# Kernel optimization log

Hardware: AMD Instinct MI355X
Metric: run time of the kernel (lower is better)

Reference implementation:

```python
import jax, jax.numpy as jnp
import numpy as np

E, H, I = 8, 1024, 512          # experts, hidden, moe_intermediate
NG, TKG, TOPK = 4, 2, 4          # n_group, topk_group, num_experts_per_tok
SCALE = 2.5                      # routed_scaling_factor


def _mlp(x, wg, wu, wd):
    # SwiGLU MLP: down(silu(gate(x)) * up(x)), all bias-free
    return (jax.nn.silu(x @ wg) * (x @ wu)) @ wd


def setup_inputs() -> dict:
    key = jax.random.key(0)
    ks = jax.random.split(key, 8)
    s = 0.02
    return {
        "hidden_states": jax.random.normal(ks[0], (32, 256, H), jnp.float32),
        "gate_w": jax.random.normal(ks[1], (E, H), jnp.float32) * np.float32(np.sqrt(2.0 / H)),
        "correction_bias": jnp.zeros((E,), jnp.float32),
        "Wg": jax.random.normal(ks[2], (E, H, I), jnp.float32) * s,
        "Wu": jax.random.normal(ks[3], (E, H, I), jnp.float32) * s,
        "Wd": jax.random.normal(ks[4], (E, I, H), jnp.float32) * s,
        "Wg_s": jax.random.normal(ks[5], (H, I), jnp.float32) * s,
        "Wu_s": jax.random.normal(ks[6], (H, I), jnp.float32) * s,
        "Wd_s": jax.random.normal(ks[7], (I, H), jnp.float32) * s,
    }


def reference(hidden_states, gate_w, correction_bias, Wg, Wu, Wd, Wg_s, Wu_s, Wd_s):
    B, T, _ = hidden_states.shape
    x = hidden_states.reshape(-1, H)                     # [N, H]
    N = x.shape[0]

    # ---- TopkRouter + route_tokens_to_experts (float32 router math) ----
    logits = x @ gate_w.T                                # [N, E]
    scores = jax.nn.sigmoid(logits)
    scores_c = scores + correction_bias                  # scores for choice
    grp = scores_c.reshape(N, NG, E // NG)
    group_scores = jnp.sum(jax.lax.top_k(grp, 2)[0], axis=-1)        # [N, NG]
    grp_idx = jax.lax.top_k(group_scores, TKG)[1]                    # [N, TKG]
    group_mask = jnp.zeros_like(group_scores).at[
        jnp.arange(N)[:, None], grp_idx].set(1.0)                    # [N, NG]
    score_mask = jnp.repeat(group_mask, E // NG, axis=-1) > 0.5      # [N, E]
    scores_for_choice = jnp.where(score_mask, scores_c, 0.0)
    topk_idx = jax.lax.top_k(scores_for_choice, TOPK)[1]             # [N, K]
    topk_w = jnp.take_along_axis(scores, topk_idx, axis=-1)          # [N, K]
    topk_w = topk_w / (jnp.sum(topk_w, axis=-1, keepdims=True) + 1e-20)
    topk_w = topk_w * SCALE

    # ---- DSNaiveMoE: equivalent dense-expert combine ----
    # combine weight per (token, expert); zero for unrouted pairs, so the
    # dense evaluation produces exactly the gather/scatter loop's result.
    cw = jnp.sum(jax.nn.one_hot(topk_idx, E, dtype=topk_w.dtype) * topk_w[..., None], axis=1)  # [N, E]
    g = jnp.einsum('nh,ehi->eni', x, Wg)
    u = jnp.einsum('nh,ehi->eni', x, Wu)
    y = jnp.einsum('eni,eih->enh', jax.nn.silu(g) * u, Wd)           # [E, N, H]
    routed = jnp.einsum('enh,ne->nh', y, cw)                          # [N, H]

    # ---- shared expert on residual input (replaces residual add) ----
    out = routed + _mlp(x, Wg_s, Wu_s, Wd_s)
    return out.reshape(B, T, H)
```

## Files before the change

### kernel.cpp

```cpp
#include <hip/hip_runtime.h>

#define E_ 8
#define H_ 1024
#define I_ 512
#define NE 9
#define NTOK 8192

typedef __bf16 bf16;
typedef __bf16 bf16x8 __attribute__((ext_vector_type(8)));
typedef __bf16 bf16x4 __attribute__((ext_vector_type(4)));
typedef float f32x4 __attribute__((ext_vector_type(4)));

__device__ __forceinline__ void gload16(const bf16* g, bf16* l) {
  __builtin_amdgcn_global_load_lds(
      (const __attribute__((address_space(1))) void*)g,
      (__attribute__((address_space(3))) void*)l,
      16, 0, 0);
}

__global__ __launch_bounds__(256) void convert_kernel(
    const float* __restrict__ x, bf16* __restrict__ xb) {
  int i = blockIdx.x * 256 + threadIdx.x;
  f32x4 v = ((const f32x4*)x)[i];
  bf16x4 o = {(bf16)v.x, (bf16)v.y, (bf16)v.z, (bf16)v.w};
  ((bf16x4*)xb)[i] = o;
}

__global__ __launch_bounds__(256) void router_kernel(
    const float* __restrict__ x, const float* __restrict__ gw,
    const float* __restrict__ bias, int4* __restrict__ topk_e,
    float4* __restrict__ topk_w) {
  int t = threadIdx.x;
  int l = t & 63, w = t >> 6;
  int n = blockIdx.x * 4 + w;
  const f32x4* xr = (const f32x4*)(x + (size_t)n * H_ + l * 16);
  float xv[16];
#pragma unroll
  for (int q = 0; q < 4; q++) {
    f32x4 v = xr[q];
    xv[q * 4 + 0] = v.x; xv[q * 4 + 1] = v.y; xv[q * 4 + 2] = v.z; xv[q * 4 + 3] = v.w;
  }
  float s[E_], sc[E_];
#pragma unroll
  for (int e = 0; e < E_; e++) {
    const f32x4* gr = (const f32x4*)(gw + e * H_ + l * 16);
    float acc = 0.f;
#pragma unroll
    for (int q = 0; q < 4; q++) {
      f32x4 g = gr[q];
      acc += xv[q * 4 + 0] * g.x + xv[q * 4 + 1] * g.y + xv[q * 4 + 2] * g.z + xv[q * 4 + 3] * g.w;
    }
#pragma unroll
    for (int off = 32; off > 0; off >>= 1) acc += __shfl_xor(acc, off, 64);
    float sig = 1.f / (1.f + __expf(-acc));
    s[e] = sig;
    sc[e] = sig + bias[e];
  }
  if (l == 0) {
    float gs[4];
#pragma unroll
    for (int g = 0; g < 4; g++) gs[g] = sc[2 * g] + sc[2 * g + 1];
    int g0 = 0;
    for (int g = 1; g < 4; g++) if (gs[g] > gs[g0]) g0 = g;
    int g1 = -1;
    for (int g = 0; g < 4; g++) {
      if (g == g0) continue;
      if (g1 < 0 || gs[g] > gs[g1]) g1 = g;
    }
    int es[4] = {2 * g0, 2 * g0 + 1, 2 * g1, 2 * g1 + 1};
    float wsum = 1e-20f;
    for (int j = 0; j < 4; j++) wsum += s[es[j]];
    float inv = 2.5f / wsum;
    topk_e[n] = (int4){es[0], es[1], es[2], es[3]};
    topk_w[n] = (float4){s[es[0]] * inv, s[es[1]] * inv, s[es[2]] * inv, s[es[3]] * inv};
  }
}

__global__ __launch_bounds__(256) void compact_kernel(
    const int4* __restrict__ topk_e, const float4* __restrict__ topk_w,
    int* __restrict__ cnt, int* __restrict__ idx, float* __restrict__ cwp) {
  __shared__ int hist[E_];
  __shared__ int base[E_];
  int t = threadIdx.x;
  if (t < E_) hist[t] = 0;
  __syncthreads();
  int n = blockIdx.x * 256 + t;
  int4 e4 = topk_e[n];
  float4 w4 = topk_w[n];
  int le[4] = {e4.x, e4.y, e4.z, e4.w};
  float lw[4] = {w4.x, w4.y, w4.z, w4.w};
  int lpos[4];
#pragma unroll
  for (int j = 0; j < 4; j++) lpos[j] = atomicAdd(&hist[le[j]], 1);
  __syncthreads();
  if (t < E_) base[t] = atomicAdd(&cnt[t], hist[t]);
  __syncthreads();
#pragma unroll
  for (int j = 0; j < 4; j++) {
    int p = base[le[j]] + lpos[j];
    idx[le[j] * NTOK + p] = n;
    cwp[le[j] * NTOK + p] = lw[j];
  }
}

__global__ __launch_bounds__(256) void transpose_kernel(
    const float* __restrict__ Wg, const float* __restrict__ Wu,
    const float* __restrict__ Wd, const float* __restrict__ Wgs,
    const float* __restrict__ Wus, const float* __restrict__ Wds,
    bf16* __restrict__ BgT, bf16* __restrict__ BuT, bf16* __restrict__ WdT) {
  __shared__ bf16 tile[32][33];
  int job = blockIdx.x >> 9;
  int tl = blockIdx.x & 511;
  const float* src;
  bf16* dst;
  int C, dst_ld;
  if (job < 18) {
    int e = job % 9;
    if (job < 9) src = (e < 8) ? Wg + (size_t)e * H_ * I_ : Wgs;
    else         src = (e < 8) ? Wu + (size_t)e * H_ * I_ : Wus;
    dst = ((job < 9) ? BgT : BuT) + (size_t)e * I_ * H_;
    C = I_; dst_ld = H_;
  } else {
    int e = job - 18;
    src = (e < 8) ? Wd + (size_t)e * I_ * H_ : Wds;
    dst = WdT + (size_t)e * H_ * I_;
    C = H_; dst_ld = I_;
  }
  int n_tc = C >> 5;
  int tr = tl / n_tc, tc = tl % n_tc;
  int tx = threadIdx.x & 31, ty = threadIdx.x >> 5;
#pragma unroll
  for (int j = 0; j < 4; j++) {
    int r = tr * 32 + ty + j * 8;
    tile[ty + j * 8][tx] = (bf16)src[(size_t)r * C + tc * 32 + tx];
  }
  __syncthreads();
#pragma unroll
  for (int j = 0; j < 4; j++) {
    int c = tc * 32 + ty + j * 8;
    dst[(size_t)c * dst_ld + tr * 32 + tx] = tile[tx][ty + j * 8];
  }
}


__global__ __launch_bounds__(256, 2) void gemm1_kernel(
    const bf16* __restrict__ X, const bf16* __restrict__ BgT,
    const bf16* __restrict__ BuT, const int* __restrict__ idx,
    const float* __restrict__ cwp, const int* __restrict__ cnt,
    bf16* __restrict__ Tc) {
  int slot = blockIdx.y;
  int e = slot >> 6;
  int m0 = (slot & 63) * 128;
  int ne = (e < 8) ? cnt[e] : NTOK;
  if (m0 >= ne) return;

  __shared__ bf16 As[128 * 64], Bgs[128 * 64], Bus[128 * 64];
  int t = threadIdx.x;
  int l = t & 63, w = t >> 6;
  int wm = w >> 1, wn = w & 1;
  int n0 = blockIdx.x * 128;

  f32x4 accg[4][4], accu[4][4];
#pragma unroll
  for (int mi = 0; mi < 4; mi++)
#pragma unroll
    for (int ni = 0; ni < 4; ni++) {
      accg[mi][ni] = (f32x4){0.f, 0.f, 0.f, 0.f};
      accu[mi][ni] = (f32x4){0.f, 0.f, 0.f, 0.f};
    }

  int srow = t >> 3;
  int scol = (((t & 7) ^ ((t >> 3) & 7)) * 8);
  int rid[4];
#pragma unroll
  for (int i = 0; i < 4; i++) {
    int r = m0 + srow + 32 * i;
    rid[i] = (e < 8) ? ((r < ne) ? idx[e * NTOK + r] : 0) : r;
  }
  const bf16* gg = BgT + (size_t)e * I_ * H_ + (size_t)(n0 + srow) * H_ + scol;
  const bf16* gu = BuT + (size_t)e * I_ * H_ + (size_t)(n0 + srow) * H_ + scol;
  bf16* la = As + w * 512;
  bf16* lg = Bgs + w * 512;
  bf16* lu = Bus + w * 512;

  for (int k0 = 0; k0 < H_; k0 += 64) {
#pragma unroll
    for (int i = 0; i < 4; i++) {
      gload16(X + (size_t)rid[i] * H_ + scol + k0, la + i * 2048);
      gload16(gg + (size_t)i * 32 * H_ + k0, lg + i * 2048);
      gload16(gu + (size_t)i * 32 * H_ + k0, lu + i * 2048);
    }
    __syncthreads();
#pragma unroll
    for (int ks = 0; ks < 2; ks++) {
      int ko = (((ks * 4 + (l >> 4)) ^ (l & 7)) * 8);
      int ar = wm * 64 + (l & 15);
      int br = wn * 64 + (l & 15);
      bf16x8 af[4], bg[4], bu[4];
#pragma unroll
      for (int mi = 0; mi < 4; mi++)
        af[mi] = *(const bf16x8*)(As + (ar + mi * 16) * 64 + ko);
#pragma unroll
      for (int ni = 0; ni < 4; ni++) {
        bg[ni] = *(const bf16x8*)(Bgs + (br + ni * 16) * 64 + ko);
        bu[ni] = *(const bf16x8*)(Bus + (br + ni * 16) * 64 + ko);
      }
#pragma unroll
      for (int mi = 0; mi < 4; mi++)
#pragma unroll
        for (int ni = 0; ni < 4; ni++) {
          accg[mi][ni] = __builtin_amdgcn_mfma_f32_16x16x32_bf16(af[mi], bg[ni], accg[mi][ni], 0, 0, 0);
          accu[mi][ni] = __builtin_amdgcn_mfma_f32_16x16x32_bf16(af[mi], bu[ni], accu[mi][ni], 0, 0, 0);
        }
    }
    __syncthreads();
  }
#pragma unroll
  for (int mi = 0; mi < 4; mi++) {
#pragma unroll
    for (int r = 0; r < 4; r++) {
      int lr = wm * 64 + mi * 16 + (l >> 4) * 4 + r;
      int pr = m0 + lr;
      if (pr < ne) {
        float c = (e < 8) ? cwp[e * NTOK + pr] : 1.0f;
#pragma unroll
        for (int ni = 0; ni < 4; ni++) {
          float g = accg[mi][ni][r];
          float u = accu[mi][ni][r];
          float val = c * (g / (1.f + __expf(-g))) * u;
          int col = n0 + wn * 64 + ni * 16 + (l & 15);
          Tc[((size_t)e * NTOK + pr) * I_ + col] = (bf16)val;
        }
      }
    }
  }
}

__global__ __launch_bounds__(256, 3) void gemm2s_kernel(
    const bf16* __restrict__ Tc, const bf16* __restrict__ WdT,
    float* __restrict__ out) {
  __shared__ bf16 As[128 * 64], Bs[128 * 64];
  int t = threadIdx.x;
  int l = t & 63, w = t >> 6;
  int wm = w >> 1, wn = w & 1;
  int m0 = blockIdx.y * 128;
  int n0 = blockIdx.x * 128;

  f32x4 acc[4][4];
#pragma unroll
  for (int mi = 0; mi < 4; mi++)
#pragma unroll
    for (int ni = 0; ni < 4; ni++) acc[mi][ni] = (f32x4){0.f, 0.f, 0.f, 0.f};

  int srow = t >> 3;
  int scol = (((t & 7) ^ ((t >> 3) & 7)) * 8);
  const bf16* ga = Tc + (size_t)8 * NTOK * I_ + (size_t)(m0 + srow) * I_ + scol;
  const bf16* gb = WdT + (size_t)8 * H_ * I_ + (size_t)(n0 + srow) * I_ + scol;
  bf16* la = As + w * 512;
  bf16* lb = Bs + w * 512;

  for (int k0 = 0; k0 < I_; k0 += 64) {
#pragma unroll
    for (int i = 0; i < 4; i++) {
      gload16(ga + (size_t)i * 32 * I_ + k0, la + i * 2048);
      gload16(gb + (size_t)i * 32 * I_ + k0, lb + i * 2048);
    }
    __syncthreads();
#pragma unroll
    for (int ks = 0; ks < 2; ks++) {
      int ko = (((ks * 4 + (l >> 4)) ^ (l & 7)) * 8);
      int ar = wm * 64 + (l & 15);
      int br = wn * 64 + (l & 15);
      bf16x8 af[4], bfv[4];
#pragma unroll
      for (int mi = 0; mi < 4; mi++)
        af[mi] = *(const bf16x8*)(As + (ar + mi * 16) * 64 + ko);
#pragma unroll
      for (int ni = 0; ni < 4; ni++)
        bfv[ni] = *(const bf16x8*)(Bs + (br + ni * 16) * 64 + ko);
#pragma unroll
      for (int mi = 0; mi < 4; mi++)
#pragma unroll
        for (int ni = 0; ni < 4; ni++)
          acc[mi][ni] = __builtin_amdgcn_mfma_f32_16x16x32_bf16(af[mi], bfv[ni], acc[mi][ni], 0, 0, 0);
    }
    __syncthreads();
  }
#pragma unroll
  for (int mi = 0; mi < 4; mi++) {
#pragma unroll
    for (int r = 0; r < 4; r++) {
      int row = m0 + wm * 64 + mi * 16 + (l >> 4) * 4 + r;
#pragma unroll
      for (int ni = 0; ni < 4; ni++) {
        int col = n0 + wn * 64 + ni * 16 + (l & 15);
        out[(size_t)row * H_ + col] = acc[mi][ni][r];
      }
    }
  }
}

__global__ __launch_bounds__(256, 3) void gemm2r_kernel(
    const bf16* __restrict__ Tc, const bf16* __restrict__ WdT,
    const int* __restrict__ idx, const int* __restrict__ cnt,
    float* __restrict__ out) {
  int slot = blockIdx.y;
  int e = slot >> 6;
  int m0 = (slot & 63) * 128;
  int ne = cnt[e];
  if (m0 >= ne) return;

  __shared__ bf16 As[128 * 64], Bs[128 * 64];
  int t = threadIdx.x;
  int l = t & 63, w = t >> 6;
  int wm = w >> 1, wn = w & 1;
  int n0 = blockIdx.x * 128;

  f32x4 acc[4][4];
#pragma unroll
  for (int mi = 0; mi < 4; mi++)
#pragma unroll
    for (int ni = 0; ni < 4; ni++) acc[mi][ni] = (f32x4){0.f, 0.f, 0.f, 0.f};

  int srow = t >> 3;
  int scol = (((t & 7) ^ ((t >> 3) & 7)) * 8);
  const bf16* ga = Tc + (size_t)e * NTOK * I_ + (size_t)(m0 + srow) * I_ + scol;
  const bf16* gb = WdT + (size_t)e * H_ * I_ + (size_t)(n0 + srow) * I_ + scol;
  bf16* la = As + w * 512;
  bf16* lb = Bs + w * 512;

  for (int k0 = 0; k0 < I_; k0 += 64) {
#pragma unroll
    for (int i = 0; i < 4; i++) {
      gload16(ga + (size_t)i * 32 * I_ + k0, la + i * 2048);
      gload16(gb + (size_t)i * 32 * I_ + k0, lb + i * 2048);
    }
    __syncthreads();
#pragma unroll
    for (int ks = 0; ks < 2; ks++) {
      int ko = (((ks * 4 + (l >> 4)) ^ (l & 7)) * 8);
      int ar = wm * 64 + (l & 15);
      int br = wn * 64 + (l & 15);
      bf16x8 af[4], bfv[4];
#pragma unroll
      for (int mi = 0; mi < 4; mi++)
        af[mi] = *(const bf16x8*)(As + (ar + mi * 16) * 64 + ko);
#pragma unroll
      for (int ni = 0; ni < 4; ni++)
        bfv[ni] = *(const bf16x8*)(Bs + (br + ni * 16) * 64 + ko);
#pragma unroll
      for (int mi = 0; mi < 4; mi++)
#pragma unroll
        for (int ni = 0; ni < 4; ni++)
          acc[mi][ni] = __builtin_amdgcn_mfma_f32_16x16x32_bf16(af[mi], bfv[ni], acc[mi][ni], 0, 0, 0);
    }
    __syncthreads();
  }
#pragma unroll
  for (int mi = 0; mi < 4; mi++) {
#pragma unroll
    for (int r = 0; r < 4; r++) {
      int lr = wm * 64 + mi * 16 + (l >> 4) * 4 + r;
      int pr = m0 + lr;
      if (pr < ne) {
        int tok = idx[e * NTOK + pr];
#pragma unroll
        for (int ni = 0; ni < 4; ni++) {
          int col = n0 + wn * 64 + ni * 16 + (l & 15);
          atomicAdd(&out[(size_t)tok * H_ + col], acc[mi][ni][r]);
        }
      }
    }
  }
}

extern "C" void kernel_launch(void* const* d_in, const int* in_sizes, int n_in,
                              void* d_out, int out_size, void* d_ws, size_t ws_size,
                              hipStream_t stream) {
  const float* x   = (const float*)d_in[0];
  const float* gw  = (const float*)d_in[1];
  const float* cb  = (const float*)d_in[2];
  const float* Wg  = (const float*)d_in[3];
  const float* Wu  = (const float*)d_in[4];
  const float* Wd  = (const float*)d_in[5];
  const float* Wgs = (const float*)d_in[6];
  const float* Wus = (const float*)d_in[7];
  const float* Wds = (const float*)d_in[8];

  char* ws = (char*)d_ws;
  size_t off = 0;
  int*    cnt    = (int*)(ws + off);    off += 64;
  int*    idx    = (int*)(ws + off);    off += (size_t)E_ * NTOK * 4;
  float*  cwp    = (float*)(ws + off);  off += (size_t)E_ * NTOK * 4;
  int4*   topk_e = (int4*)(ws + off);   off += (size_t)NTOK * 16;
  float4* topk_w = (float4*)(ws + off); off += (size_t)NTOK * 16;
  bf16* BgT = (bf16*)(ws + off);  off += (size_t)NE * I_ * H_ * 2;
  bf16* BuT = (bf16*)(ws + off);  off += (size_t)NE * I_ * H_ * 2;
  bf16* WdT = (bf16*)(ws + off);  off += (size_t)NE * H_ * I_ * 2;
  bf16* Xb  = (bf16*)(ws + off);  off += (size_t)NTOK * H_ * 2;
  bf16* Tc  = (bf16*)(ws + off);  off += (size_t)NE * NTOK * I_ * 2;

  hipMemsetAsync(cnt, 0, 64, stream);
  hipLaunchKernelGGL(convert_kernel, dim3(NTOK * H_ / 1024), dim3(256), 0, stream,
                     x, Xb);
  hipLaunchKernelGGL(transpose_kernel, dim3(27 * 512), dim3(256), 0, stream,
                     Wg, Wu, Wd, Wgs, Wus, Wds, BgT, BuT, WdT);
  hipLaunchKernelGGL(router_kernel, dim3(NTOK / 4), dim3(256), 0, stream,
                     x, gw, cb, topk_e, topk_w);
  hipLaunchKernelGGL(compact_kernel, dim3(NTOK / 256), dim3(256), 0, stream,
                     topk_e, topk_w, cnt, idx, cwp);
  hipLaunchKernelGGL(gemm1_kernel, dim3(4, NE * 64), dim3(256), 0, stream,
                     Xb, BgT, BuT, idx, cwp, cnt, Tc);
  hipLaunchKernelGGL(gemm2s_kernel, dim3(8, 64), dim3(256), 0, stream,
                     Tc, WdT, (float*)d_out);
  hipLaunchKernelGGL(gemm2r_kernel, dim3(8, E_ * 64), dim3(256), 0, stream,
                     Tc, WdT, idx, cnt, (float*)d_out);
}
```

Measured before the change: 422.4 us.

## Replace atomic scatter in routed down-projection with bf16 staging and gather-combine kernel

The routed down-projection now writes per-expert results as bf16 into a compacted staging buffer instead of atomically adding fp32 values into the output. A new combine kernel reads each token's four expert rows through a token-position map built in the compaction step and adds them to the shared-expert output. This removes 32M scattered float atomics. In exchange it adds an extra pass over a 64MB buffer and rounds the routed contributions to bf16 before summation.

```diff
diff --git a/kernel.cpp b/kernel.cpp
--- a/kernel.cpp
+++ b/kernel.cpp
@@ -78,7 +78,8 @@
 
 __global__ __launch_bounds__(256) void compact_kernel(
     const int4* __restrict__ topk_e, const float4* __restrict__ topk_w,
-    int* __restrict__ cnt, int* __restrict__ idx, float* __restrict__ cwp) {
+    int* __restrict__ cnt, int* __restrict__ idx, float* __restrict__ cwp,
+    int* __restrict__ tokpos) {
   __shared__ int hist[E_];
   __shared__ int base[E_];
   int t = threadIdx.x;
@@ -100,6 +101,7 @@
     int p = base[le[j]] + lpos[j];
     idx[le[j] * NTOK + p] = n;
     cwp[le[j] * NTOK + p] = lw[j];
+    tokpos[n * 4 + j] = (le[j] << 13) | p;
   }
 }
 
@@ -302,13 +304,14 @@
 
 __global__ __launch_bounds__(256, 3) void gemm2r_kernel(
     const bf16* __restrict__ Tc, const bf16* __restrict__ WdT,
-    const int* __restrict__ idx, const int* __restrict__ cnt,
-    float* __restrict__ out) {
+    const int* __restrict__ cnt, bf16* __restrict__ Yp) {
   int slot = blockIdx.y;
   int e = slot >> 6;
   int m0 = (slot & 63) * 128;
   int ne = cnt[e];
   if (m0 >= ne) return;
+  int off_e = 0;
+  for (int ee = 0; ee < e; ee++) off_e += cnt[ee];
 
   __shared__ bf16 As[128 * 64], Bs[128 * 64];
   int t = threadIdx.x;
@@ -363,15 +366,40 @@
       int lr = wm * 64 + mi * 16 + (l >> 4) * 4 + r;
       int pr = m0 + lr;
       if (pr < ne) {
-        int tok = idx[e * NTOK + pr];
 #pragma unroll
         for (int ni = 0; ni < 4; ni++) {
           int col = n0 + wn * 64 + ni * 16 + (l & 15);
-          atomicAdd(&out[(size_t)tok * H_ + col], acc[mi][ni][r]);
+          Yp[(size_t)(off_e + pr) * H_ + col] = (bf16)acc[mi][ni][r];
         }
       }
     }
   }
+}
+
+__global__ __launch_bounds__(256) void combine_kernel(
+    const int* __restrict__ cnt, const int* __restrict__ tokpos,
+    const bf16* __restrict__ Yp, float* __restrict__ out) {
+  int t = threadIdx.x;
+  int tok = blockIdx.x * 2 + (t >> 7);
+  int cb = (t & 127) * 8;
+  int off[E_];
+  int a = 0;
+#pragma unroll
+  for (int e = 0; e < E_; e++) { off[e] = a; a += cnt[e]; }
+  float* op = out + (size_t)tok * H_ + cb;
+  f32x4 o0 = *(const f32x4*)(op);
+  f32x4 o1 = *(const f32x4*)(op + 4);
+  float sum[8] = {o0.x, o0.y, o0.z, o0.w, o1.x, o1.y, o1.z, o1.w};
+#pragma unroll
+  for (int j = 0; j < 4; j++) {
+    int tp = tokpos[tok * 4 + j];
+    int e = tp >> 13, p = tp & 8191;
+    bf16x8 v = *(const bf16x8*)(Yp + (size_t)(off[e] + p) * H_ + cb);
+#pragma unroll
+    for (int q = 0; q < 8; q++) sum[q] += (float)v[q];
+  }
+  *(f32x4*)(op) = (f32x4){sum[0], sum[1], sum[2], sum[3]};
+  *(f32x4*)(op + 4) = (f32x4){sum[4], sum[5], sum[6], sum[7]};
 }
 
 extern "C" void kernel_launch(void* const* d_in, const int* in_sizes, int n_in,
@@ -394,11 +422,13 @@
   float*  cwp    = (float*)(ws + off);  off += (size_t)E_ * NTOK * 4;
   int4*   topk_e = (int4*)(ws + off);   off += (size_t)NTOK * 16;
   float4* topk_w = (float4*)(ws + off); off += (size_t)NTOK * 16;
+  int*    tokpos = (int*)(ws + off);    off += (size_t)NTOK * 4 * 4;
   bf16* BgT = (bf16*)(ws + off);  off += (size_t)NE * I_ * H_ * 2;
   bf16* BuT = (bf16*)(ws + off);  off += (size_t)NE * I_ * H_ * 2;
   bf16* WdT = (bf16*)(ws + off);  off += (size_t)NE * H_ * I_ * 2;
   bf16* Xb  = (bf16*)(ws + off);  off += (size_t)NTOK * H_ * 2;
   bf16* Tc  = (bf16*)(ws + off);  off += (size_t)NE * NTOK * I_ * 2;
+  bf16* Yp  = (bf16*)(ws + off);  off += (size_t)4 * NTOK * H_ * 2;
 
   hipMemsetAsync(cnt, 0, 64, stream);
   hipLaunchKernelGGL(convert_kernel, dim3(NTOK * H_ / 1024), dim3(256), 0, stream,
@@ -408,11 +438,13 @@
   hipLaunchKernelGGL(router_kernel, dim3(NTOK / 4), dim3(256), 0, stream,
                      x, gw, cb, topk_e, topk_w);
   hipLaunchKernelGGL(compact_kernel, dim3(NTOK / 256), dim3(256), 0, stream,
-                     topk_e, topk_w, cnt, idx, cwp);
+                     topk_e, topk_w, cnt, idx, cwp, tokpos);
   hipLaunchKernelGGL(gemm1_kernel, dim3(4, NE * 64), dim3(256), 0, stream,
                      Xb, BgT, BuT, idx, cwp, cnt, Tc);
   hipLaunchKernelGGL(gemm2s_kernel, dim3(8, 64), dim3(256), 0, stream,
                      Tc, WdT, (float*)d_out);
   hipLaunchKernelGGL(gemm2r_kernel, dim3(8, E_ * 64), dim3(256), 0, stream,
-                     Tc, WdT, idx, cnt, (float*)d_out);
-}
+                     Tc, WdT, cnt, Yp);
+  hipLaunchKernelGGL(combine_kernel, dim3(NTOK / 2), dim3(256), 0, stream,
+                     cnt, tokpos, Yp, (float*)d_out);
+}
```

Result: faster. 387.9 us (-8.2%).
